# Kernel optimization log

Hardware: AMD Instinct MI355X
Metric: run time of the kernel (lower is better)

The kernel has to match this reference:

```python
import jax, jax.numpy as jnp
import numpy as np

D_MODEL = 1024
N_HEADS = 16
D_K = D_MODEL // N_HEADS
B, S = 4, 2048


def setup_inputs() -> dict:
    key = jax.random.key(0)
    ks = jax.random.split(key, 9)
    sc = 1.0 / np.sqrt(D_MODEL)
    return {
        "x": jax.random.normal(ks[0], (B, S, D_MODEL), dtype=jnp.float32),
        "Wq": jax.random.normal(ks[1], (D_MODEL, D_MODEL), dtype=jnp.float32) * sc,
        "bq": jax.random.normal(ks[2], (D_MODEL,), dtype=jnp.float32) * 0.02,
        "Wk": jax.random.normal(ks[3], (D_MODEL, D_MODEL), dtype=jnp.float32) * sc,
        "bk": jax.random.normal(ks[4], (D_MODEL,), dtype=jnp.float32) * 0.02,
        "Wv": jax.random.normal(ks[5], (D_MODEL, D_MODEL), dtype=jnp.float32) * sc,
        "bv": jax.random.normal(ks[6], (D_MODEL,), dtype=jnp.float32) * 0.02,
        "Wo": jax.random.normal(ks[7], (D_MODEL, D_MODEL), dtype=jnp.float32) * sc,
        "bo": jax.random.normal(ks[8], (D_MODEL,), dtype=jnp.float32) * 0.02,
    }


def reference(x, Wq, bq, Wk, bk, Wv, bv, Wo, bo):
    b, s, _ = x.shape
    # QKV projections (torch Linear: x @ W.T + b; here weights are stored as [in, out])
    q = (x @ Wq + bq).reshape(b, s, N_HEADS, D_K).transpose(0, 2, 1, 3)  # [b,h,s,dk]
    k = (x @ Wk + bk).reshape(b, s, N_HEADS, D_K).transpose(0, 2, 1, 3)
    v = (x @ Wv + bv).reshape(b, s, N_HEADS, D_K).transpose(0, 2, 1, 3)
    scores = jnp.einsum("bhqd,bhkd->bhqk", q, k) / jnp.sqrt(jnp.float32(D_K))
    attn = jax.nn.softmax(scores, axis=-1)  # dropout=0.0 -> identity
    out = jnp.einsum("bhqk,bhkd->bhqd", attn, v)
    out = out.transpose(0, 2, 1, 3).reshape(b, s, D_MODEL)
    return out @ Wo + bo
```

## Files before the change

kernel.cpp:

```cpp
#include <hip/hip_runtime.h>
#include <hip/hip_bf16.h>

#define DM    1024
#define NH    16
#define DKH   64
#define BB    4
#define SS    2048
#define MROWS (BB*SS)
#define NQKV  (3*DM)

typedef __attribute__((ext_vector_type(8))) __bf16 bf16x8;
typedef __attribute__((ext_vector_type(4))) float f32x4;
typedef __attribute__((ext_vector_type(16))) float f32x16;
typedef __attribute__((ext_vector_type(4))) unsigned short u16x4;

__device__ __forceinline__ void gload_lds16(const void* g, void* l) {
  __builtin_amdgcn_global_load_lds((const __attribute__((address_space(1))) void*)g,
                                   (__attribute__((address_space(3))) void*)l, 16, 0, 0);
}

__device__ __forceinline__ unsigned short f2bf(float f) {
  __hip_bfloat16 h = __float2bfloat16(f);
  unsigned short u;
  __builtin_memcpy(&u, &h, 2);
  return u;
}

__device__ __forceinline__ unsigned pack2(float a, float b) {
  return (unsigned)f2bf(a) | ((unsigned)f2bf(b) << 16);
}


__global__ __launch_bounds__(256) void cvt_bf16_kernel(const float* __restrict__ in,
                                                       unsigned short* __restrict__ out, int n4) {
  int i = blockIdx.x * 256 + threadIdx.x;
  if (i >= n4) return;
  float4 v = reinterpret_cast<const float4*>(in)[i];
  u16x4 o = { f2bf(v.x), f2bf(v.y), f2bf(v.z), f2bf(v.w) };
  reinterpret_cast<u16x4*>(out)[i] = o;
}

__global__ __launch_bounds__(256) void transpose_cvt4_kernel(
    const float* __restrict__ Wq, const float* __restrict__ Wk,
    const float* __restrict__ Wv, const float* __restrict__ Wo,
    unsigned short* __restrict__ WTqkv, unsigned short* __restrict__ WTo) {
  const int z = blockIdx.z;
  const float* W = (z == 0) ? Wq : (z == 1) ? Wk : (z == 2) ? Wv : Wo;
  unsigned short* WT = (z == 3) ? WTo : (WTqkv + (long)z * DM * DM);
  __shared__ float t[32][33];
  int tx = threadIdx.x & 31, ty = threadIdx.x >> 5;
  int bx = blockIdx.x * 32, by = blockIdx.y * 32;
#pragma unroll
  for (int i = 0; i < 32; i += 8)
    t[ty + i][tx] = W[(long)(by + ty + i) * DM + bx + tx];
  __syncthreads();
#pragma unroll
  for (int i = 0; i < 32; i += 8)
    WT[(long)(bx + ty + i) * DM + by + tx] = f2bf(t[tx][ty + i]);
}

__global__ void concat3_bias_kernel(const float* __restrict__ a, const float* __restrict__ b,
                                    const float* __restrict__ c, float* __restrict__ out) {
  int i = blockIdx.x * 256 + threadIdx.x;
  if (i >= NQKV) return;
  out[i] = (i < DM) ? a[i] : (i < 2 * DM) ? b[i - DM] : c[i - 2 * DM];
}


template <int MODE>
__global__ __launch_bounds__(256) void gemm_bt_kernel(
    const unsigned short* __restrict__ A,
    const unsigned short* __restrict__ BT,
    const float* __restrict__ bias,
    void* __restrict__ out0, void* __restrict__ out1, void* __restrict__ out2,
    int M, int N, int K) {
  __shared__ unsigned short As[128 * 32];
  __shared__ unsigned short Bs[128 * 32];
  const int tid = threadIdx.x;
  const int lane = tid & 63;
  const int lr = lane & 15, lg = lane >> 4;
  const int wv = tid >> 6, wm = wv >> 1, wn = wv & 1;
  const long bm = blockIdx.x, bn = blockIdx.y;

  const unsigned short* Ag = A + bm * 128 * K;
  const unsigned short* Bg = BT + bn * 128 * K;

  f32x4 acc[4][4];
#pragma unroll
  for (int i = 0; i < 4; ++i)
#pragma unroll
    for (int j = 0; j < 4; ++j) acc[i][j] = (f32x4){0.f, 0.f, 0.f, 0.f};

  for (int kt = 0; kt < K; kt += 32) {
#pragma unroll
    for (int it = 0; it < 2; ++it) {
      const int e = it * 2048 + tid * 8;
      const int row = e >> 5, col = e & 31;
      gload_lds16(Ag + (long)row * K + kt + col, As + e);
      gload_lds16(Bg + (long)row * K + kt + col, Bs + e);
    }
    __syncthreads();
    bf16x8 af[4], bfr[4];
#pragma unroll
    for (int mi = 0; mi < 4; ++mi)
      af[mi] = *reinterpret_cast<const bf16x8*>(As + (wm * 64 + mi * 16 + lr) * 32 + lg * 8);
#pragma unroll
    for (int ni = 0; ni < 4; ++ni)
      bfr[ni] = *reinterpret_cast<const bf16x8*>(Bs + (wn * 64 + ni * 16 + lr) * 32 + lg * 8);
#pragma unroll
    for (int mi = 0; mi < 4; ++mi)
#pragma unroll
      for (int ni = 0; ni < 4; ++ni)
        acc[mi][ni] = __builtin_amdgcn_mfma_f32_16x16x32_bf16(af[mi], bfr[ni], acc[mi][ni], 0, 0, 0);
    __syncthreads();
  }

  const float QSC = 0.125f * 1.44269504088896340736f;
#pragma unroll
  for (int ni = 0; ni < 4; ++ni) {
    const int col = (int)bn * 128 + wn * 64 + ni * 16 + lr;
    const float bc = bias[col];
#pragma unroll
    for (int mi = 0; mi < 4; ++mi) {
      const int row0 = (int)bm * 128 + wm * 64 + mi * 16 + lg * 4;
#pragma unroll
      for (int r = 0; r < 4; ++r) {
        const int row = row0 + r;
        float v = acc[mi][ni][r] + bc;
        if (MODE == 0) {
          if (col < DM) {
            ((unsigned short*)out0)[(long)row * DM + col] = f2bf(v * QSC);
          } else if (col < 2 * DM) {
            const int c2 = col - DM;
            const int h = c2 >> 6, dh = c2 & 63;
            const int b = row >> 11, s = row & 2047;
            const long idx = ((((long)(b * NH + h) * 32 + (s >> 6)) * 512 +
                               (dh >> 3) * 64 + (s & 63)) << 3) + (dh & 7);
            ((unsigned short*)out1)[idx] = f2bf(v);
          } else {
            const int c2 = col - 2 * DM;
            const int h = c2 >> 6, dh = c2 & 63;
            const int b = row >> 11, s = row & 2047;
            const long idx = ((((long)(b * NH + h) * 32 + (s >> 6)) * 512 +
                               ((s >> 3) & 7) * 64 + dh) << 3) + (s & 7);
            ((unsigned short*)out2)[idx] = f2bf(v);
          }
        } else {
          ((float*)out0)[(long)row * (long)N + col] = v;
        }
      }
    }
  }
}


__global__ __launch_bounds__(256, 3) void attn_kernel(
    const unsigned short* __restrict__ Qb,
    const unsigned short* __restrict__ Kf,
    const unsigned short* __restrict__ Vf,
    unsigned short* __restrict__ AO) {
  __shared__ __align__(16) unsigned short sK[2][4096];
  __shared__ __align__(16) unsigned short sV[2][4096];

  const int tid = threadIdx.x;
  const int lane = tid & 63;
  const int wv = tid >> 6;
  const int q5 = lane & 31;
  const int hi = lane >> 5;

  const int bh = blockIdx.x;
  const int qt = blockIdx.y;
  const int b = bh >> 4, h = bh & 15;

  bf16x8 qf[4];
  {
    const unsigned short* qrow = Qb + (long)(b * SS + qt * 128 + wv * 32 + q5) * DM + h * DKH;
#pragma unroll
    for (int dstep = 0; dstep < 4; ++dstep)
      qf[dstep] = *reinterpret_cast<const bf16x8*>(qrow + dstep * 16 + hi * 8);
  }

  const unsigned short* Kp = Kf + (long)bh * 32 * 4096;
  const unsigned short* Vp = Vf + (long)bh * 32 * 4096;

  f32x16 accv[2];
#pragma unroll
  for (int d = 0; d < 2; ++d)
#pragma unroll
    for (int r = 0; r < 16; ++r) accv[d][r] = 0.f;
  f32x16 lacc;
#pragma unroll
  for (int r = 0; r < 16; ++r) lacc[r] = 0.f;

  f32x16 zc;
#pragma unroll
  for (int r = 0; r < 16; ++r) zc[r] = 0.f;

  auto stage = [&](int buf, int t) {
#pragma unroll
    for (int it = 0; it < 2; ++it) {
      const int u = it * 256 + tid;
      gload_lds16(Kp + (long)t * 4096 + u * 8, &sK[buf][u * 8]);
      gload_lds16(Vp + (long)t * 4096 + u * 8, &sV[buf][u * 8]);
    }
  };

  stage(0, 0);
  __syncthreads();

#pragma unroll 1
  for (int kt = 0; kt < SS / 64; ++kt) {
    const int cur = kt & 1;
    if (kt + 1 < SS / 64) stage(cur ^ 1, kt + 1);
    const unsigned short* K_ = sK[cur];
    const unsigned short* V_ = sV[cur];

    f32x16 s4[2];
    __builtin_amdgcn_s_setprio(1);
#pragma unroll
    for (int kb = 0; kb < 2; ++kb)
#pragma unroll
      for (int dstep = 0; dstep < 4; ++dstep) {
        bf16x8 kf = *reinterpret_cast<const bf16x8*>(
            K_ + ((dstep * 2 + hi) * 64 + kb * 32 + q5) * 8);
        s4[kb] = __builtin_amdgcn_mfma_f32_32x32x16_bf16(kf, qf[dstep],
                                                         dstep ? s4[kb] : zc, 0, 0, 0);
      }
    __builtin_amdgcn_s_setprio(0);

#pragma unroll
    for (int kb = 0; kb < 2; ++kb)
#pragma unroll
      for (int r = 0; r < 16; ++r)
        s4[kb][r] = __builtin_amdgcn_exp2f(s4[kb][r]);
#pragma unroll
    for (int r = 0; r < 16; ++r) lacc[r] += s4[0][r] + s4[1][r];

#pragma unroll
    for (int step = 0; step < 4; ++step) {
      const int kb = step >> 1, rb = (step & 1) * 8;
      unsigned w0, w1, w2, w3;
      asm("v_cvt_pk_bf16_f32 %0, %1, %2" : "=v"(w0) : "v"(s4[kb][rb + 0]), "v"(s4[kb][rb + 1]));
      asm("v_cvt_pk_bf16_f32 %0, %1, %2" : "=v"(w1) : "v"(s4[kb][rb + 2]), "v"(s4[kb][rb + 3]));
      asm("v_cvt_pk_bf16_f32 %0, %1, %2" : "=v"(w2) : "v"(s4[kb][rb + 4]), "v"(s4[kb][rb + 5]));
      asm("v_cvt_pk_bf16_f32 %0, %1, %2" : "=v"(w3) : "v"(s4[kb][rb + 6]), "v"(s4[kb][rb + 7]));
      const unsigned c = hi ? w0 : w2;
      const unsigned d = hi ? w1 : w3;
      const unsigned xc = (unsigned)__shfl_xor((int)c, 32);
      const unsigned xd = (unsigned)__shfl_xor((int)d, 32);
      union { unsigned u[4]; bf16x8 v; } pf;
      pf.u[0] = hi ? xc : w0;
      pf.u[1] = hi ? xd : w1;
      pf.u[2] = hi ? w2 : xc;
      pf.u[3] = hi ? w3 : xd;
      __builtin_amdgcn_s_setprio(1);
#pragma unroll
      for (int dblk = 0; dblk < 2; ++dblk) {
        bf16x8 vf = *reinterpret_cast<const bf16x8*>(
            V_ + ((step * 2 + hi) * 64 + dblk * 32 + q5) * 8);
        accv[dblk] = __builtin_amdgcn_mfma_f32_32x32x16_bf16(vf, pf.v, accv[dblk], 0, 0, 0);
      }
      __builtin_amdgcn_s_setprio(0);
    }
    __syncthreads();
  }

  float l01 = (lacc[0] + lacc[1]) + (lacc[2] + lacc[3]);
  float l23 = (lacc[4] + lacc[5]) + (lacc[6] + lacc[7]);
  float l45 = (lacc[8] + lacc[9]) + (lacc[10] + lacc[11]);
  float l67 = (lacc[12] + lacc[13]) + (lacc[14] + lacc[15]);
  float l = (l01 + l23) + (l45 + l67);
  l += __shfl_xor(l, 32);
  const float inv = 1.0f / l;

  const long row = (long)b * SS + qt * 128 + wv * 32 + q5;
  unsigned short* orow = AO + row * DM + h * DKH;
#pragma unroll
  for (int dblk = 0; dblk < 2; ++dblk)
#pragma unroll
    for (int j = 0; j < 8; ++j) {
      const int d0 = dblk * 32 + 8 * (j >> 1) + 4 * hi + 2 * (j & 1);
      const unsigned w = pack2(accv[dblk][2 * j] * inv, accv[dblk][2 * j + 1] * inv);
      *reinterpret_cast<unsigned*>(orow + d0) = w;
    }
}


extern "C" void kernel_launch(void* const* d_in, const int* in_sizes, int n_in,
                              void* d_out, int out_size, void* d_ws, size_t ws_size,
                              hipStream_t stream) {
  const float* x  = (const float*)d_in[0];
  const float* Wq = (const float*)d_in[1];
  const float* bq = (const float*)d_in[2];
  const float* Wk = (const float*)d_in[3];
  const float* bk = (const float*)d_in[4];
  const float* Wv = (const float*)d_in[5];
  const float* bv = (const float*)d_in[6];
  const float* Wo = (const float*)d_in[7];
  const float* bo = (const float*)d_in[8];
  float* out = (float*)d_out;

  char* ws = (char*)d_ws;
  size_t off = 0;
  auto alloc = [&](size_t bytes) {
    void* p = ws + off;
    off += (bytes + 255) & ~(size_t)255;
    return p;
  };
  unsigned short* Xb    = (unsigned short*)alloc((size_t)MROWS * DM * 2);
  unsigned short* WTqkv = (unsigned short*)alloc((size_t)3 * DM * DM * 2);
  unsigned short* WTo   = (unsigned short*)alloc((size_t)DM * DM * 2);
  float*          bqkv  = (float*)alloc((size_t)NQKV * 4);
  unsigned short* Qb    = (unsigned short*)alloc((size_t)MROWS * DM * 2);
  unsigned short* Kb2   = (unsigned short*)alloc((size_t)MROWS * DM * 2);
  unsigned short* Vb2   = (unsigned short*)alloc((size_t)MROWS * DM * 2);
  unsigned short* AOb   = (unsigned short*)alloc((size_t)MROWS * DM * 2);

  cvt_bf16_kernel<<<(MROWS * DM / 4 + 255) / 256, 256, 0, stream>>>(x, Xb, MROWS * DM / 4);
  transpose_cvt4_kernel<<<dim3(32, 32, 4), 256, 0, stream>>>(Wq, Wk, Wv, Wo, WTqkv, WTo);
  concat3_bias_kernel<<<(NQKV + 255) / 256, 256, 0, stream>>>(bq, bk, bv, bqkv);

  gemm_bt_kernel<0><<<dim3(MROWS / 128, NQKV / 128), 256, 0, stream>>>(
      Xb, WTqkv, bqkv, Qb, Kb2, Vb2, MROWS, NQKV, DM);

  attn_kernel<<<dim3(BB * NH, SS / 128), 256, 0, stream>>>(Qb, Kb2, Vb2, AOb);

  gemm_bt_kernel<2><<<dim3(MROWS / 128, DM / 128), 256, 0, stream>>>(
      AOb, WTo, bo, out, nullptr, nullptr, MROWS, DM, DM);
}
```

Before: 232.3 us.

## Double-buffer GEMM LDS loads and use permlane32 swap in attention

The GEMM kernel now keeps two LDS stages and issues the global-to-LDS loads for tile t+2 while computing tile t. It uses explicit vmcnt waits and barriers, and raises wave priority around the MFMA block, so load latency is hidden behind compute. In the attention kernel, the shuffle-based half-wave exchange of packed P fragments is replaced with v_permlane32_swap, which removes the ds_bpermute traffic and selects. The output bf16 packing now uses a single v_cvt_pk_bf16_f32 instead of two scalar conversions. The GEMM uses more LDS per block, which may reduce occupancy, and the hand-written waitcnt logic has to stay correct.

```diff
diff --git a/kernel.cpp b/kernel.cpp
--- a/kernel.cpp
+++ b/kernel.cpp
@@ -26,8 +26,10 @@
   return u;
 }
 
-__device__ __forceinline__ unsigned pack2(float a, float b) {
-  return (unsigned)f2bf(a) | ((unsigned)f2bf(b) << 16);
+__device__ __forceinline__ unsigned cvtpk2(float a, float b) {
+  unsigned w;
+  asm("v_cvt_pk_bf16_f32 %0, %1, %2" : "=v"(w) : "v"(a), "v"(b));
+  return w;
 }
 
 
@@ -74,8 +76,7 @@
     const float* __restrict__ bias,
     void* __restrict__ out0, void* __restrict__ out1, void* __restrict__ out2,
     int M, int N, int K) {
-  __shared__ unsigned short As[128 * 32];
-  __shared__ unsigned short Bs[128 * 32];
+  __shared__ __align__(16) unsigned short smem[16384];
   const int tid = threadIdx.x;
   const int lane = tid & 63;
   const int lr = lane & 15, lg = lane >> 4;
@@ -91,28 +92,54 @@
 #pragma unroll
     for (int j = 0; j < 4; ++j) acc[i][j] = (f32x4){0.f, 0.f, 0.f, 0.f};
 
-  for (int kt = 0; kt < K; kt += 32) {
+  auto issue = [&](int buf, int kt) {
 #pragma unroll
     for (int it = 0; it < 2; ++it) {
       const int e = it * 2048 + tid * 8;
       const int row = e >> 5, col = e & 31;
-      gload_lds16(Ag + (long)row * K + kt + col, As + e);
-      gload_lds16(Bg + (long)row * K + kt + col, Bs + e);
-    }
-    __syncthreads();
+      gload_lds16(Ag + (long)row * K + kt * 32 + col, smem + buf * 4096 + e);
+      gload_lds16(Bg + (long)row * K + kt * 32 + col, smem + 8192 + buf * 4096 + e);
+    }
+  };
+
+  const int NT = K / 32;
+  issue(0, 0);
+  issue(1, 1);
+  asm volatile("s_waitcnt vmcnt(4)" ::: "memory");
+  __builtin_amdgcn_s_barrier();
+
+  for (int t = 0; t < NT; ++t) {
+    const int buf = t & 1;
+    const unsigned short* As_ = smem + buf * 4096;
+    const unsigned short* Bs_ = smem + 8192 + buf * 4096;
+
     bf16x8 af[4], bfr[4];
 #pragma unroll
     for (int mi = 0; mi < 4; ++mi)
-      af[mi] = *reinterpret_cast<const bf16x8*>(As + (wm * 64 + mi * 16 + lr) * 32 + lg * 8);
+      af[mi] = *reinterpret_cast<const bf16x8*>(As_ + (wm * 64 + mi * 16 + lr) * 32 + lg * 8);
 #pragma unroll
     for (int ni = 0; ni < 4; ++ni)
-      bfr[ni] = *reinterpret_cast<const bf16x8*>(Bs + (wn * 64 + ni * 16 + lr) * 32 + lg * 8);
+      bfr[ni] = *reinterpret_cast<const bf16x8*>(Bs_ + (wn * 64 + ni * 16 + lr) * 32 + lg * 8);
+    __builtin_amdgcn_s_setprio(1);
 #pragma unroll
     for (int mi = 0; mi < 4; ++mi)
 #pragma unroll
       for (int ni = 0; ni < 4; ++ni)
         acc[mi][ni] = __builtin_amdgcn_mfma_f32_16x16x32_bf16(af[mi], bfr[ni], acc[mi][ni], 0, 0, 0);
-    __syncthreads();
+    __builtin_amdgcn_s_setprio(0);
+
+    if (t + 1 < NT) {
+      asm volatile("s_waitcnt lgkmcnt(0)" ::: "memory");
+      __builtin_amdgcn_s_barrier();
+      if (t + 2 < NT) {
+        issue(buf, t + 2);
+        asm volatile("s_waitcnt vmcnt(4)" ::: "memory");
+      } else {
+        asm volatile("s_waitcnt vmcnt(0)" ::: "memory");
+      }
+      __builtin_amdgcn_s_barrier();
+      asm volatile("" ::: "memory");
+    }
   }
 
   const float QSC = 0.125f * 1.44269504088896340736f;
@@ -244,15 +271,13 @@
       asm("v_cvt_pk_bf16_f32 %0, %1, %2" : "=v"(w1) : "v"(s4[kb][rb + 2]), "v"(s4[kb][rb + 3]));
       asm("v_cvt_pk_bf16_f32 %0, %1, %2" : "=v"(w2) : "v"(s4[kb][rb + 4]), "v"(s4[kb][rb + 5]));
       asm("v_cvt_pk_bf16_f32 %0, %1, %2" : "=v"(w3) : "v"(s4[kb][rb + 6]), "v"(s4[kb][rb + 7]));
-      const unsigned c = hi ? w0 : w2;
-      const unsigned d = hi ? w1 : w3;
-      const unsigned xc = (unsigned)__shfl_xor((int)c, 32);
-      const unsigned xd = (unsigned)__shfl_xor((int)d, 32);
+      asm("v_permlane32_swap_b32 %0, %1" : "+v"(w0), "+v"(w2));
+      asm("v_permlane32_swap_b32 %0, %1" : "+v"(w1), "+v"(w3));
       union { unsigned u[4]; bf16x8 v; } pf;
-      pf.u[0] = hi ? xc : w0;
-      pf.u[1] = hi ? xd : w1;
-      pf.u[2] = hi ? w2 : xc;
-      pf.u[3] = hi ? w3 : xd;
+      pf.u[0] = w0;
+      pf.u[1] = w1;
+      pf.u[2] = w2;
+      pf.u[3] = w3;
       __builtin_amdgcn_s_setprio(1);
 #pragma unroll
       for (int dblk = 0; dblk < 2; ++dblk) {
@@ -280,7 +305,7 @@
 #pragma unroll
     for (int j = 0; j < 8; ++j) {
       const int d0 = dblk * 32 + 8 * (j >> 1) + 4 * hi + 2 * (j & 1);
-      const unsigned w = pack2(accv[dblk][2 * j] * inv, accv[dblk][2 * j + 1] * inv);
+      const unsigned w = cvtpk2(accv[dblk][2 * j] * inv, accv[dblk][2 * j + 1] * inv);
       *reinterpret_cast<unsigned*>(orow + d0) = w;
     }
 }
```

Result: faster. 221.7 us, median of 4 (-4.5%).
